# Kernel optimization log

Hardware: AMD Instinct MI355X
Metric: run time of the kernel (lower is better)

## Reference

```python
import jax, jax.numpy as jnp
import numpy as np

B, L, D, H, NL, C = 8, 512, 64, 256, 2, 8
EPS = 1e-5
NEG = -1e9


def _causal_softmax(scores):
    # scores: (B, L, L); lower-triangular causal mask then softmax over last dim
    Ls = scores.shape[-1]
    mask = jnp.tril(jnp.ones((Ls, Ls), dtype=bool))
    return jax.nn.softmax(jnp.where(mask, scores, NEG), axis=-1)


def _attn_plain(x):
    s = jnp.einsum('bld,bmd->blm', x, x)
    return jnp.einsum('blm,bmd->bld', _causal_softmax(s), x)


def _attn_sdpa(x):
    s = jnp.einsum('bld,bmd->blm', x, x) / jnp.sqrt(jnp.float32(x.shape[-1]))
    return jnp.einsum('blm,bmd->bld', _causal_softmax(s), x)


def _attn_additive(x):
    # materializes (B, L, L, D) as in the original module
    s = jnp.tanh(x[:, :, None, :] + x[:, None, :, :]).sum(axis=-1)  # (B,L,L)
    return jnp.einsum('blm,bmd->bld', _causal_softmax(s), x)


def _bn(x, gamma, beta):
    # training-mode BatchNorm1d over (B, L) per feature; x: (B, L, F)
    mu = x.mean(axis=(0, 1))
    var = ((x - mu) ** 2).mean(axis=(0, 1))
    return (x - mu) * jax.lax.rsqrt(var + EPS) * gamma + beta


def _lstm_layer(x, Wih, Whh, bih, bhh):
    # x: (B, L, K) -> (B, L, H). PyTorch gate order: i, f, g, o.
    Hh = Whh.shape[1]
    xg = jnp.einsum('blk,gk->blg', x, Wih) + bih + bhh  # (B, L, 4H)
    xg = jnp.swapaxes(xg, 0, 1)  # (L, B, 4H)

    def step(carry, xt):
        h, c = carry
        g = xt + h @ Whh.T
        i = jax.nn.sigmoid(g[:, 0 * Hh:1 * Hh])
        f = jax.nn.sigmoid(g[:, 1 * Hh:2 * Hh])
        gg = jnp.tanh(g[:, 2 * Hh:3 * Hh])
        o = jax.nn.sigmoid(g[:, 3 * Hh:4 * Hh])
        c = f * c + i * gg
        h = o * jnp.tanh(c)
        return (h, c), h

    h0 = jnp.zeros((x.shape[0], Hh), x.dtype)
    _, hs = jax.lax.scan(step, (h0, h0), xg)
    return jnp.swapaxes(hs, 0, 1)  # (B, L, H)


def setup_inputs() -> dict:
    key = jax.random.key(0)
    ks = jax.random.split(key, 20)
    s = 1.0 / np.sqrt(H)
    u = lambda k, sh: jax.random.uniform(k, sh, jnp.float32, -s, s)
    return {
        'src': jax.random.normal(ks[0], (B, L, D), jnp.float32),
        'attn_w': jax.random.uniform(ks[1], (3, L, D), jnp.float32, 0.5, 1.5),
        'cat_w': jax.random.uniform(ks[2], (3, L, H), jnp.float32, 0.5, 1.5),
        'bn1_gamma': 1.0 + 0.1 * jax.random.normal(ks[3], (3, D), jnp.float32),
        'bn1_beta': 0.1 * jax.random.normal(ks[4], (3, D), jnp.float32),
        'bn2_gamma': 1.0 + 0.1 * jax.random.normal(ks[5], (H,), jnp.float32),
        'bn2_beta': 0.1 * jax.random.normal(ks[6], (H,), jnp.float32),
        'Wih0': u(ks[7], (3, 4 * H, D)),
        'Whh0': u(ks[8], (3, 4 * H, H)),
        'bih0': u(ks[9], (3, 4 * H)),
        'bhh0': u(ks[10], (3, 4 * H)),
        'Wih1': u(ks[11], (3, 4 * H, H)),
        'Whh1': u(ks[12], (3, 4 * H, H)),
        'bih1': u(ks[13], (3, 4 * H)),
        'bhh1': u(ks[14], (3, 4 * H)),
        'fc_W': u(ks[15], (C, H)),
        'fc_b': u(ks[16], (C,)),
    }


def reference(src, attn_w, cat_w, bn1_gamma, bn1_beta, bn2_gamma, bn2_beta,
              Wih0, Whh0, bih0, bhh0, Wih1, Whh1, bih1, bhh1, fc_W, fc_b):
    # three attentions, normalized weighted sum
    outs = jnp.stack([_attn_plain(src), _attn_additive(src), _attn_sdpa(src)])  # (3,B,L,D)
    aw = attn_w / attn_w.sum(axis=0)  # (3, L, D)
    attention_output = jnp.einsum('kbld,kld->bld', outs, aw)

    line1 = _bn(src, bn1_gamma[0], bn1_beta[0])
    line2 = _bn(src + attention_output, bn1_gamma[1], bn1_beta[1])
    line3 = _bn(attention_output, bn1_gamma[2], bn1_beta[2])

    def lstm2(x, i):
        h = _lstm_layer(x, Wih0[i], Whh0[i], bih0[i], bhh0[i])
        return _lstm_layer(h, Wih1[i], Whh1[i], bih1[i], bhh1[i])

    l1 = lstm2(line1, 0)
    l2 = lstm2(line2, 1)
    l3 = lstm2(line3, 2)

    cw = cat_w / cat_w.sum(axis=0)  # (3, L, H)
    cat = l1 * cw[0] + l2 * cw[1] + l3 * cw[2]
    cat = _bn(cat, bn2_gamma, bn2_beta)
    # eval-mode dropout is identity
    return cat[:, -1, :] @ fc_W.T + fc_b  # (B, C)
```

## Files before the change

kernel.cpp:

```cpp
#include <hip/hip_runtime.h>

#define B_ 8
#define L_ 512
#define D_ 64
#define H_ 256
#define GH 1024
#define EPS_ 1e-5f
#define POISON_ 0xAAAAAAAAu

typedef float f32x4 __attribute__((ext_vector_type(4)));
typedef _Float16 half8 __attribute__((ext_vector_type(8)));

__device__ __forceinline__ unsigned short f2h(float f) {
  _Float16 h = (_Float16)f;
  return __builtin_bit_cast(unsigned short, h);
}
__device__ __forceinline__ float h2f(unsigned short s) {
  _Float16 h = __builtin_bit_cast(_Float16, s);
  return (float)h;
}
__device__ __forceinline__ float fast_tanh(float x) {
  return 1.0f - 2.0f / (1.0f + __expf(2.0f * x));
}
__device__ __forceinline__ float fast_sig(float x) {
  return 1.0f / (1.0f + __expf(-x));
}
__device__ __forceinline__ unsigned int load_agent(const unsigned int* p) {
  return __hip_atomic_load(p, __ATOMIC_RELAXED, __HIP_MEMORY_SCOPE_AGENT);
}

__global__ void scores_kernel(const float* __restrict__ src,
                              float* __restrict__ Sp, float* __restrict__ Sa) {
  const int l = blockIdx.x, b = blockIdx.y;
  __shared__ float xl[D_];
  if (threadIdx.x < D_) xl[threadIdx.x] = src[(b * L_ + l) * D_ + threadIdx.x];
  __syncthreads();
  for (int m = threadIdx.x; m <= l; m += blockDim.x) {
    const float4* xr = (const float4*)&src[(b * L_ + m) * D_];
    float dp = 0.f, da = 0.f;
#pragma unroll
    for (int d4 = 0; d4 < D_ / 4; ++d4) {
      float4 v = xr[d4];
      dp += xl[d4*4+0]*v.x + xl[d4*4+1]*v.y + xl[d4*4+2]*v.z + xl[d4*4+3]*v.w;
      da += fast_tanh(xl[d4*4+0]+v.x) + fast_tanh(xl[d4*4+1]+v.y)
          + fast_tanh(xl[d4*4+2]+v.z) + fast_tanh(xl[d4*4+3]+v.w);
    }
    Sp[(b * L_ + l) * L_ + m] = dp;
    Sa[(b * L_ + l) * L_ + m] = da;
  }
}

__global__ void softmax_av_kernel(const float* __restrict__ src, const float* __restrict__ Sp,
                                  const float* __restrict__ Sa, float* __restrict__ outk) {
  const int l = blockIdx.x, b = blockIdx.y, k = blockIdx.z;
  const int lane = threadIdx.x;
  __shared__ float p[L_];
  const float* row = (k == 1) ? &Sa[(b * L_ + l) * L_] : &Sp[(b * L_ + l) * L_];
  const float scale = (k == 2) ? 0.125f : 1.0f;
  float mx = -1e30f;
  for (int m = lane; m <= l; m += 64) { float v = row[m] * scale; p[m] = v; mx = fmaxf(mx, v); }
#pragma unroll
  for (int off = 32; off > 0; off >>= 1) mx = fmaxf(mx, __shfl_xor(mx, off, 64));
  float sum = 0.f;
  for (int m = lane; m <= l; m += 64) { float e = __expf(p[m] - mx); p[m] = e; sum += e; }
#pragma unroll
  for (int off = 32; off > 0; off >>= 1) sum += __shfl_xor(sum, off, 64);
  __syncthreads();
  const float inv = 1.0f / sum;
  float acc = 0.f;
  for (int m = 0; m <= l; ++m) acc += p[m] * src[(b * L_ + m) * D_ + lane];
  outk[((k * B_ + b) * L_ + l) * D_ + lane] = acc * inv;
}

__global__ void combine_kernel(const float* __restrict__ outk, const float* __restrict__ attn_w,
                               float* __restrict__ attn) {
  int i = blockIdx.x * blockDim.x + threadIdx.x;
  if (i >= B_ * L_ * D_) return;
  int ld = i & (L_ * D_ - 1);
  float w0 = attn_w[ld], w1 = attn_w[L_ * D_ + ld], w2 = attn_w[2 * L_ * D_ + ld];
  float o0 = outk[i], o1 = outk[B_ * L_ * D_ + i], o2 = outk[2 * B_ * L_ * D_ + i];
  attn[i] = (o0 * w0 + o1 * w1 + o2 * w2) / (w0 + w1 + w2);
}

__global__ void bn1_kernel(const float* __restrict__ src, const float* __restrict__ attn,
                           const float* __restrict__ gamma, const float* __restrict__ beta,
                           float* __restrict__ line_in) {
  const int d = blockIdx.x, line = blockIdx.y;
  float s1 = 0.f, s2 = 0.f;
  for (int i = threadIdx.x; i < B_ * L_; i += blockDim.x) {
    float v = (line == 0) ? src[i * D_ + d]
            : (line == 1) ? src[i * D_ + d] + attn[i * D_ + d]
                          : attn[i * D_ + d];
    s1 += v; s2 += v * v;
  }
#pragma unroll
  for (int off = 32; off > 0; off >>= 1) { s1 += __shfl_xor(s1, off, 64); s2 += __shfl_xor(s2, off, 64); }
  __shared__ float a1[4], a2[4];
  __shared__ float mean_s, rstd_s;
  int w = threadIdx.x >> 6;
  if ((threadIdx.x & 63) == 0) { a1[w] = s1; a2[w] = s2; }
  __syncthreads();
  if (threadIdx.x == 0) {
    float t1 = a1[0] + a1[1] + a1[2] + a1[3];
    float t2 = a2[0] + a2[1] + a2[2] + a2[3];
    float mean = t1 / (float)(B_ * L_);
    float var = t2 / (float)(B_ * L_) - mean * mean;
    mean_s = mean; rstd_s = rsqrtf(var + EPS_);
  }
  __syncthreads();
  const float mean = mean_s;
  const float gs = gamma[line * D_ + d] * rstd_s, be = beta[line * D_ + d];
  for (int i = threadIdx.x; i < B_ * L_; i += blockDim.x) {
    float v = (line == 0) ? src[i * D_ + d]
            : (line == 1) ? src[i * D_ + d] + attn[i * D_ + d]
                          : attn[i * D_ + d];
    line_in[line * B_ * L_ * D_ + i * D_ + d] = (v - mean) * gs + be;
  }
}

template <int IN_K>
__device__ __forceinline__ void rec_body(
    const float* __restrict__ in_f32,
    const unsigned short* __restrict__ in_b16,
    const float* __restrict__ Wih, const float* __restrict__ Whh,
    const float* __restrict__ bih, const float* __restrict__ bhh,
    unsigned short* __restrict__ hseq,
    int line, int s,
    unsigned short* hprev, unsigned short* inbuf,
    float (*gbuf)[32][8], float (*biasS)[32]) {
  constexpr int INROW = IN_K + 8;
  constexpr int NKT_IN = IN_K / 32;
  const int tid = threadIdx.x, w = tid >> 6, lane = tid & 63;
  const int q = lane >> 4, col = lane & 15;

  half8 whhF[2][8];
  half8 wihF[2][NKT_IN];
#pragma unroll
  for (int T = 0; T < 2; ++T) {
    const int n = w * H_ + s * 32 + T * 16 + col;
    const float* wr = &Whh[(line * GH + n) * H_];
#pragma unroll
    for (int kt = 0; kt < 8; ++kt) {
      const float* pk = wr + kt * 32 + q * 8;
      half8 t;
#pragma unroll
      for (int j = 0; j < 8; ++j) t[j] = (_Float16)pk[j];
      whhF[T][kt] = t;
    }
    const float* wr2 = &Wih[(line * GH + n) * IN_K];
#pragma unroll
    for (int kt = 0; kt < NKT_IN; ++kt) {
      const float* pk = wr2 + kt * 32 + q * 8;
      half8 t;
#pragma unroll
      for (int j = 0; j < 8; ++j) t[j] = (_Float16)pk[j];
      wihF[T][kt] = t;
    }
  }
  if (tid < 128) {
    int g = tid >> 5, j = tid & 31;
    int n = g * H_ + s * 32 + j;
    biasS[g][j] = bih[line * GH + n] + bhh[line * GH + n];
  }
  for (int i = tid; i < 16 * 264; i += 256) hprev[i] = 0;
  for (int i = tid; i < 16 * INROW; i += 256) inbuf[i] = 0;

  const unsigned int* gaddr_base[4];
  int gdst[4];
  bool gremote[4];
#pragma unroll
  for (int rr = 0; rr < 4; ++rr) {
    int u = tid + rr * 256;
    int r = u >> 7, v = u & 127, b = v >> 4, pz = v & 15;
    int cidx = r * 32 + pz * 2;
    gremote[rr] = (r != s);
    gdst[rr] = b * 264 + cidx;
    gaddr_base[rr] = (const unsigned int*)&hseq[(size_t)(line * L_) * B_ * H_ + b * H_ + cidx];
  }

  auto stage = [&](int t) {
    if constexpr (IN_K == 64) {
      float v0 = in_f32[(line * B_ * L_ + (tid >> 6) * L_ + t) * D_ + (tid & 63)];
      float v1 = in_f32[(line * B_ * L_ + ((tid + 256) >> 6) * L_ + t) * D_ + (tid & 63)];
      inbuf[(tid >> 6) * INROW + (tid & 63)] = f2h(v0);
      inbuf[((tid + 256) >> 6) * INROW + (tid & 63)] = f2h(v1);
    } else {
      const unsigned int* sa[4];
      unsigned int sv[4];
#pragma unroll
      for (int r = 0; r < 4; ++r) {
        int u = tid + r * 256;
        int b = u >> 7, pr = u & 127;
        sa[r] = (const unsigned int*)&in_b16[((line * L_ + t) * B_ + b) * H_ + pr * 2];
        sv[r] = load_agent(sa[r]);
      }
#pragma unroll
      for (int r = 0; r < 4; ++r) {
        unsigned int x = sv[r];
        while (x == POISON_) x = load_agent(sa[r]);
        int u = tid + r * 256;
        int b = u >> 7, pr = u & 127;
        *(unsigned int*)&inbuf[b * INROW + pr * 2] = x;
      }
    }
  };

  stage(0);
  float c0 = 0.f, c1 = 0.f;
  const int ub = tid & 7, jp = (tid >> 3) * 2;
  __syncthreads();

  for (int t = 0; t < L_; ++t) {
    f32x4 acc0 = {0.f, 0.f, 0.f, 0.f}, acc1 = {0.f, 0.f, 0.f, 0.f};
#pragma unroll
    for (int kt = 0; kt < NKT_IN; ++kt) {
      half8 a = *(const half8*)&inbuf[col * INROW + kt * 32 + q * 8];
      acc0 = __builtin_amdgcn_mfma_f32_16x16x32_f16(a, wihF[0][kt], acc0, 0, 0, 0);
      acc1 = __builtin_amdgcn_mfma_f32_16x16x32_f16(a, wihF[1][kt], acc1, 0, 0, 0);
    }
#pragma unroll
    for (int kt = 0; kt < 8; ++kt) {
      half8 a = *(const half8*)&hprev[col * 264 + kt * 32 + q * 8];
      acc0 = __builtin_amdgcn_mfma_f32_16x16x32_f16(a, whhF[0][kt], acc0, 0, 0, 0);
      acc1 = __builtin_amdgcn_mfma_f32_16x16x32_f16(a, whhF[1][kt], acc1, 0, 0, 0);
    }
    if (q < 2) {
#pragma unroll
      for (int r = 0; r < 4; ++r) {
        gbuf[w][col][q * 4 + r] = acc0[r];
        gbuf[w][16 + col][q * 4 + r] = acc1[r];
      }
    }
    __syncthreads();

    if (tid < 128) {
      float gi0 = gbuf[0][jp][ub] + biasS[0][jp];
      float gf0 = gbuf[1][jp][ub] + biasS[1][jp];
      float gg0 = gbuf[2][jp][ub] + biasS[2][jp];
      float go0 = gbuf[3][jp][ub] + biasS[3][jp];
      float gi1 = gbuf[0][jp+1][ub] + biasS[0][jp+1];
      float gf1 = gbuf[1][jp+1][ub] + biasS[1][jp+1];
      float gg1 = gbuf[2][jp+1][ub] + biasS[2][jp+1];
      float go1 = gbuf[3][jp+1][ub] + biasS[3][jp+1];
      c0 = fast_sig(gf0) * c0 + fast_sig(gi0) * fast_tanh(gg0);
      c1 = fast_sig(gf1) * c1 + fast_sig(gi1) * fast_tanh(gg1);
      float h0 = fast_sig(go0) * fast_tanh(c0);
      float h1 = fast_sig(go1) * fast_tanh(c1);
      unsigned int packed = (unsigned int)f2h(h0) | ((unsigned int)f2h(h1) << 16);
      if (packed == POISON_) packed ^= 1u;
      __hip_atomic_store(
          (unsigned int*)&hseq[((line * L_ + t) * B_ + ub) * H_ + s * 32 + jp],
          packed, __ATOMIC_RELAXED, __HIP_MEMORY_SCOPE_AGENT);
      *(unsigned int*)&hprev[ub * 264 + s * 32 + jp] = packed;
    }

    if (t == L_ - 1) break;

    unsigned int gv[4];
    const unsigned int* ga[4];
#pragma unroll
    for (int rr = 0; rr < 4; ++rr) {
      ga[rr] = gaddr_base[rr] + (size_t)t * (B_ * H_ / 2) -
               0;
      ga[rr] = (const unsigned int*)((const unsigned short*)gaddr_base[rr] + (size_t)t * B_ * H_);
      gv[rr] = gremote[rr] ? load_agent(ga[rr]) : 0u;
    }
    stage(t + 1);
#pragma unroll
    for (int rr = 0; rr < 4; ++rr) {
      if (gremote[rr]) {
        unsigned int x = gv[rr];
        while (x == POISON_) x = load_agent(ga[rr]);
        *(unsigned int*)&hprev[gdst[rr]] = x;
      }
    }
    __syncthreads();
  }
}

__global__ __launch_bounds__(256, 1) void rec_fused_kernel(
    const float* __restrict__ line_in,
    const float* __restrict__ Wih0, const float* __restrict__ Whh0,
    const float* __restrict__ bih0, const float* __restrict__ bhh0,
    const float* __restrict__ Wih1, const float* __restrict__ Whh1,
    const float* __restrict__ bih1, const float* __restrict__ bhh1,
    unsigned short* __restrict__ hseq0, unsigned short* __restrict__ hseq1) {
  __shared__ unsigned short hprev[16 * 264];
  __shared__ unsigned short inbuf[16 * 264];
  __shared__ float gbuf[4][32][8];
  __shared__ float biasS[4][32];
  const int blk = blockIdx.x;
  const int layer = blk / 24, rem = blk % 24;
  const int line = rem >> 3, s = rem & 7;
  if (layer == 0)
    rec_body<64>(line_in, nullptr, Wih0, Whh0, bih0, bhh0, hseq0,
                 line, s, hprev, inbuf, gbuf, biasS);
  else
    rec_body<256>(nullptr, hseq0, Wih1, Whh1, bih1, bhh1, hseq1,
                  line, s, hprev, inbuf, gbuf, biasS);
}

__global__ void bn2stats_kernel(const unsigned short* __restrict__ hseq1,
                                const float* __restrict__ cat_w, float* __restrict__ stats) {
  const int h = blockIdx.x;
  float s1 = 0.f, s2 = 0.f;
  for (int i = threadIdx.x; i < B_ * L_; i += blockDim.x) {
    int l = i >> 3, b = i & 7;
    float w0 = cat_w[(0 * L_ + l) * H_ + h], w1 = cat_w[(1 * L_ + l) * H_ + h],
          w2 = cat_w[(2 * L_ + l) * H_ + h];
    float v0 = h2f(hseq1[((0 * L_ + l) * B_ + b) * H_ + h]);
    float v1 = h2f(hseq1[((1 * L_ + l) * B_ + b) * H_ + h]);
    float v2 = h2f(hseq1[((2 * L_ + l) * B_ + b) * H_ + h]);
    float v = (v0 * w0 + v1 * w1 + v2 * w2) / (w0 + w1 + w2);
    s1 += v; s2 += v * v;
  }
#pragma unroll
  for (int off = 32; off > 0; off >>= 1) { s1 += __shfl_xor(s1, off, 64); s2 += __shfl_xor(s2, off, 64); }
  __shared__ float a1[4], a2[4];
  int w = threadIdx.x >> 6;
  if ((threadIdx.x & 63) == 0) { a1[w] = s1; a2[w] = s2; }
  __syncthreads();
  if (threadIdx.x == 0) {
    float t1 = a1[0] + a1[1] + a1[2] + a1[3];
    float t2 = a2[0] + a2[1] + a2[2] + a2[3];
    float mean = t1 / (float)(B_ * L_);
    float var = t2 / (float)(B_ * L_) - mean * mean;
    stats[2 * h] = mean;
    stats[2 * h + 1] = rsqrtf(var + EPS_);
  }
}

__global__ void final_kernel(const unsigned short* __restrict__ hseq1,
                             const float* __restrict__ cat_w, const float* __restrict__ stats,
                             const float* __restrict__ gamma, const float* __restrict__ beta,
                             const float* __restrict__ fcW, const float* __restrict__ fcb,
                             float* __restrict__ out) {
  const int h = threadIdx.x;
  __shared__ float vmat[B_][H_];
  const float mean = stats[2 * h], rstd = stats[2 * h + 1];
  const float g = gamma[h], be = beta[h];
  const int l = L_ - 1;
  float w0 = cat_w[(0 * L_ + l) * H_ + h], w1 = cat_w[(1 * L_ + l) * H_ + h],
        w2 = cat_w[(2 * L_ + l) * H_ + h];
  const float wsum = w0 + w1 + w2;
  for (int b = 0; b < B_; ++b) {
    float v0 = h2f(hseq1[((0 * L_ + l) * B_ + b) * H_ + h]);
    float v1 = h2f(hseq1[((1 * L_ + l) * B_ + b) * H_ + h]);
    float v2 = h2f(hseq1[((2 * L_ + l) * B_ + b) * H_ + h]);
    float v = (v0 * w0 + v1 * w1 + v2 * w2) / wsum;
    vmat[b][h] = (v - mean) * rstd * g + be;
  }
  __syncthreads();
  if (h < 64) {
    int b = h >> 3, c = h & 7;
    float acc = fcb[c];
    for (int k = 0; k < H_; ++k) acc += vmat[b][k] * fcW[c * H_ + k];
    out[b * 8 + c] = acc;
  }
}

extern "C" void kernel_launch(void* const* d_in, const int* in_sizes, int n_in,
                              void* d_out, int out_size, void* d_ws, size_t ws_size,
                              hipStream_t stream) {
  (void)in_sizes; (void)n_in; (void)out_size; (void)ws_size;
  const float* src       = (const float*)d_in[0];
  const float* attn_w    = (const float*)d_in[1];
  const float* cat_w     = (const float*)d_in[2];
  const float* bn1_gamma = (const float*)d_in[3];
  const float* bn1_beta  = (const float*)d_in[4];
  const float* bn2_gamma = (const float*)d_in[5];
  const float* bn2_beta  = (const float*)d_in[6];
  const float* Wih0      = (const float*)d_in[7];
  const float* Whh0      = (const float*)d_in[8];
  const float* bih0      = (const float*)d_in[9];
  const float* bhh0      = (const float*)d_in[10];
  const float* Wih1      = (const float*)d_in[11];
  const float* Whh1      = (const float*)d_in[12];
  const float* bih1      = (const float*)d_in[13];
  const float* bhh1      = (const float*)d_in[14];
  const float* fcW       = (const float*)d_in[15];
  const float* fcb       = (const float*)d_in[16];
  float* out = (float*)d_out;

  char* p = (char*)d_ws;
  float* Sp = (float*)p;                      p += (size_t)B_ * L_ * L_ * 4;
  float* Sa = (float*)p;                      p += (size_t)B_ * L_ * L_ * 4;
  float* outk = (float*)p;                    p += (size_t)3 * B_ * L_ * D_ * 4;
  float* attn = (float*)p;                    p += (size_t)B_ * L_ * D_ * 4;
  float* line_in = (float*)p;                 p += (size_t)3 * B_ * L_ * D_ * 4;
  float* stats = (float*)p;                   p += (size_t)512 * 4;
  unsigned short* hseq0 = (unsigned short*)p; p += (size_t)3 * L_ * B_ * H_ * 2;
  unsigned short* hseq1 = (unsigned short*)p; p += (size_t)3 * L_ * B_ * H_ * 2;

  scores_kernel<<<dim3(L_, B_), dim3(256), 0, stream>>>(src, Sp, Sa);
  softmax_av_kernel<<<dim3(L_, B_, 3), dim3(64), 0, stream>>>(src, Sp, Sa, outk);
  combine_kernel<<<dim3((B_ * L_ * D_) / 256), dim3(256), 0, stream>>>(outk, attn_w, attn);
  bn1_kernel<<<dim3(D_, 3), dim3(256), 0, stream>>>(src, attn, bn1_gamma, bn1_beta, line_in);
  rec_fused_kernel<<<dim3(48), dim3(256), 0, stream>>>(
      line_in, Wih0, Whh0, bih0, bhh0, Wih1, Whh1, bih1, bhh1, hseq0, hseq1);
  bn2stats_kernel<<<dim3(H_), dim3(256), 0, stream>>>(hseq1, cat_w, stats);
  final_kernel<<<dim3(1), dim3(256), 0, stream>>>(hseq1, cat_w, stats, bn2_gamma, bn2_beta,
                                                  fcW, fcb, out);
}
```

Before: 1.410 ms.

## Co-locate each LSTM group on one XCD and poll hidden state with L2-scope loads

Remaps block indices so that all eight slices of a given (line, layer) recurrence share the same blockIdx mod 8, which places them on one XCD under round-robin dispatch. The grid grows to 62 blocks, and the two unused residues exit early. Cross-block hidden-state exchange now uses inline-asm sc0 global loads and stores that are meant to be served from the shared L2 instead of device-scope coherent memory. Loads fall back to agent-scope loads every few spins, and stores are issued twice. This relies on hardware dispatch order and cache-scope behaviour for correctness and speed, and the extra store adds traffic.

```diff
diff --git a/kernel.cpp b/kernel.cpp
--- a/kernel.cpp
+++ b/kernel.cpp
@@ -27,6 +27,30 @@
 }
 __device__ __forceinline__ unsigned int load_agent(const unsigned int* p) {
   return __hip_atomic_load(p, __ATOMIC_RELAXED, __HIP_MEMORY_SCOPE_AGENT);
+}
+__device__ __forceinline__ unsigned int load_se(const unsigned int* p) {
+  unsigned int v;
+  asm volatile("global_load_dword %0, %1, off sc0\n\ts_waitcnt vmcnt(0)"
+               : "=&v"(v) : "v"(p) : "memory");
+  return v;
+}
+__device__ __forceinline__ void load_se4(const unsigned int* p0, const unsigned int* p1,
+                                         const unsigned int* p2, const unsigned int* p3,
+                                         unsigned int& v0, unsigned int& v1,
+                                         unsigned int& v2, unsigned int& v3) {
+  asm volatile(
+      "global_load_dword %0, %4, off sc0\n\t"
+      "global_load_dword %1, %5, off sc0\n\t"
+      "global_load_dword %2, %6, off sc0\n\t"
+      "global_load_dword %3, %7, off sc0\n\t"
+      "s_waitcnt vmcnt(0)"
+      : "=&v"(v0), "=&v"(v1), "=&v"(v2), "=&v"(v3)
+      : "v"(p0), "v"(p1), "v"(p2), "v"(p3)
+      : "memory");
+}
+__device__ __forceinline__ void store_h_dual(unsigned int* p, unsigned int v) {
+  asm volatile("global_store_dword %0, %1, off sc0" :: "v"(p), "v"(v) : "memory");
+  __hip_atomic_store(p, v, __ATOMIC_RELAXED, __HIP_MEMORY_SCOPE_AGENT);
 }
 
 __global__ void scores_kernel(const float* __restrict__ src,
@@ -165,9 +189,9 @@
   for (int i = tid; i < 16 * 264; i += 256) hprev[i] = 0;
   for (int i = tid; i < 16 * INROW; i += 256) inbuf[i] = 0;
 
-  const unsigned int* gaddr_base[4];
   int gdst[4];
   bool gremote[4];
+  int goff[4];
 #pragma unroll
   for (int rr = 0; rr < 4; ++rr) {
     int u = tid + rr * 256;
@@ -175,7 +199,7 @@
     int cidx = r * 32 + pz * 2;
     gremote[rr] = (r != s);
     gdst[rr] = b * 264 + cidx;
-    gaddr_base[rr] = (const unsigned int*)&hseq[(size_t)(line * L_) * B_ * H_ + b * H_ + cidx];
+    goff[rr] = b * H_ + cidx;
   }
 
   auto stage = [&](int t) {
@@ -248,29 +272,29 @@
       float h1 = fast_sig(go1) * fast_tanh(c1);
       unsigned int packed = (unsigned int)f2h(h0) | ((unsigned int)f2h(h1) << 16);
       if (packed == POISON_) packed ^= 1u;
-      __hip_atomic_store(
-          (unsigned int*)&hseq[((line * L_ + t) * B_ + ub) * H_ + s * 32 + jp],
-          packed, __ATOMIC_RELAXED, __HIP_MEMORY_SCOPE_AGENT);
+      store_h_dual(
+          (unsigned int*)&hseq[((line * L_ + t) * B_ + ub) * H_ + s * 32 + jp], packed);
       *(unsigned int*)&hprev[ub * 264 + s * 32 + jp] = packed;
     }
 
     if (t == L_ - 1) break;
 
+    const unsigned short* hrow = &hseq[(size_t)(line * L_ + t) * B_ * H_];
+    const unsigned int* ga[4];
     unsigned int gv[4];
-    const unsigned int* ga[4];
-#pragma unroll
-    for (int rr = 0; rr < 4; ++rr) {
-      ga[rr] = gaddr_base[rr] + (size_t)t * (B_ * H_ / 2) -
-               0;
-      ga[rr] = (const unsigned int*)((const unsigned short*)gaddr_base[rr] + (size_t)t * B_ * H_);
-      gv[rr] = gremote[rr] ? load_agent(ga[rr]) : 0u;
-    }
+#pragma unroll
+    for (int rr = 0; rr < 4; ++rr) ga[rr] = (const unsigned int*)(hrow + goff[rr]);
+    load_se4(ga[0], ga[1], ga[2], ga[3], gv[0], gv[1], gv[2], gv[3]);
     stage(t + 1);
 #pragma unroll
     for (int rr = 0; rr < 4; ++rr) {
       if (gremote[rr]) {
         unsigned int x = gv[rr];
-        while (x == POISON_) x = load_agent(ga[rr]);
+        int spin = 0;
+        while (x == POISON_) {
+          x = load_se(ga[rr]);
+          if (x == POISON_ && ((++spin & 3) == 3)) x = load_agent(ga[rr]);
+        }
         *(unsigned int*)&hprev[gdst[rr]] = x;
       }
     }
@@ -289,9 +313,10 @@
   __shared__ unsigned short inbuf[16 * 264];
   __shared__ float gbuf[4][32][8];
   __shared__ float biasS[4][32];
-  const int blk = blockIdx.x;
-  const int layer = blk / 24, rem = blk % 24;
-  const int line = rem >> 3, s = rem & 7;
+  const int g = blockIdx.x & 7;
+  if (g >= 6) return;
+  const int s = blockIdx.x >> 3;
+  const int line = g >> 1, layer = g & 1;
   if (layer == 0)
     rec_body<64>(line_in, nullptr, Wih0, Whh0, bih0, bhh0, hseq0,
                  line, s, hprev, inbuf, gbuf, biasS);
@@ -396,7 +421,7 @@
   softmax_av_kernel<<<dim3(L_, B_, 3), dim3(64), 0, stream>>>(src, Sp, Sa, outk);
   combine_kernel<<<dim3((B_ * L_ * D_) / 256), dim3(256), 0, stream>>>(outk, attn_w, attn);
   bn1_kernel<<<dim3(D_, 3), dim3(256), 0, stream>>>(src, attn, bn1_gamma, bn1_beta, line_in);
-  rec_fused_kernel<<<dim3(48), dim3(256), 0, stream>>>(
+  rec_fused_kernel<<<dim3(62), dim3(256), 0, stream>>>(
       line_in, Wih0, Whh0, bih0, bhh0, Wih1, Whh1, bih1, bhh1, hseq0, hseq1);
   bn2stats_kernel<<<dim3(H_), dim3(256), 0, stream>>>(hseq1, cat_w, stats);
   final_kernel<<<dim3(1), dim3(256), 0, stream>>>(hseq1, cat_w, stats, bn2_gamma, bn2_beta,
```

Result: slower. 1.983 ms (+40.7%).
